# Kernel tuning notes

Measured on AMD Instinct MI355X. Metric: run time of the kernel, lower is better.

Reference implementation:

```python
import jax, jax.numpy as jnp
import numpy as np

N_NODES = 10000
N_EDGES = 80000
OBS_DIMS = 128
HIDDEN = 1024
ACT_DIMS = 8
N_GRAPHS = 64


def setup_inputs() -> dict:
    key = jax.random.key(0)
    ks = jax.random.split(key, 8)
    x = jax.random.normal(ks[0], (N_NODES, OBS_DIMS), dtype=jnp.float32)
    edge_index = jax.random.randint(ks[1], (2, N_EDGES), 0, N_NODES, dtype=jnp.int64)
    batch = jnp.sort(jax.random.randint(ks[2], (N_NODES,), 0, N_GRAPHS, dtype=jnp.int64))
    # Glorot-style init for weights, zero bias (as in PyG GCNConv / Linear defaults)
    W1 = jax.random.normal(ks[3], (OBS_DIMS, HIDDEN), dtype=jnp.float32) * (1.0 / np.sqrt(OBS_DIMS))
    b1 = jnp.zeros((HIDDEN,), dtype=jnp.float32)
    W2 = jax.random.normal(ks[4], (HIDDEN, HIDDEN), dtype=jnp.float32) * (1.0 / np.sqrt(HIDDEN))
    b2 = jnp.zeros((HIDDEN,), dtype=jnp.float32)
    Wl = jax.random.normal(ks[5], (HIDDEN, ACT_DIMS), dtype=jnp.float32) * (1.0 / np.sqrt(HIDDEN))
    bl = jnp.zeros((ACT_DIMS,), dtype=jnp.float32)
    return {"x": x, "edge_index": edge_index, "batch": batch,
            "W1": W1, "b1": b1, "W2": W2, "b2": b2, "Wl": Wl, "bl": bl}


def _gcn_conv(x, src, dst, dinv, W, b, n):
    """PyG GCNConv: D^-1/2 (A+I) D^-1/2 X W + b (self-loops already in src/dst)."""
    h = x @ W                                   # [N, out]
    norm = (dinv[src] * dinv[dst])[:, None]      # [E+N, 1]
    msg = h[src] * norm                          # gather + scale
    out = jax.ops.segment_sum(msg, dst, num_segments=n)
    return out + b


def reference(x, edge_index, batch, W1, b1, W2, b2, Wl, bl):
    n = x.shape[0]
    loops = jnp.arange(n, dtype=edge_index.dtype)
    src = jnp.concatenate([edge_index[0], loops])  # add self-loops
    dst = jnp.concatenate([edge_index[1], loops])
    # degree (with self-loops) from destination column, as PyG does
    deg = jax.ops.segment_sum(jnp.ones_like(dst, dtype=x.dtype), dst, num_segments=n)
    dinv = jax.lax.rsqrt(jnp.maximum(deg, 1.0))

    h = jax.nn.relu(_gcn_conv(x, src, dst, dinv, W1, b1, n))
    h = _gcn_conv(h, src, dst, dinv, W2, b2, n)
    h = jnp.tanh(h @ Wl + bl)                    # [N, act_dims]

    # global_mean_pool over batch segment ids
    sums = jax.ops.segment_sum(h, batch, num_segments=N_GRAPHS)
    counts = jax.ops.segment_sum(jnp.ones((n, 1), h.dtype), batch, num_segments=N_GRAPHS)
    return sums / jnp.maximum(counts, 1.0)       # [N_GRAPHS, act_dims]
```

## Files before the change

### kernel.cpp

```cpp
#include <hip/hip_runtime.h>
#include <hip/hip_bf16.h>

#define NNODES 10000
#define NEDGES 80000
#define OBS    128
#define HID    1024
#define ACTD   8
#define NGR    64

typedef __bf16 bf16x8 __attribute__((ext_vector_type(8)));
typedef float  f32x4  __attribute__((ext_vector_type(4)));
typedef const __attribute__((address_space(1))) unsigned int gl_u32;
typedef __attribute__((address_space(3))) unsigned int lds_u32;

__device__ __forceinline__ ushort f2b(float f) {
    union { float f; unsigned int i; } v; v.f = f;
    unsigned int lsb = (v.i >> 16) & 1u;
    unsigned int r = v.i + 0x7fffu + lsb;
    return (ushort)(r >> 16);
}
__device__ __forceinline__ int cix(int v, int hi) {
    return v < 0 ? 0 : (v >= hi ? hi - 1 : v);
}

__global__ __launch_bounds__(256) void k_prep(const float* __restrict__ W1,
                                              const float* __restrict__ W2,
                                              const float* __restrict__ Wl,
                                              const float* __restrict__ b2,
                                              const float* __restrict__ bl,
                                              ushort* __restrict__ Wt1,
                                              ushort* __restrict__ M2bf,
                                              float* __restrict__ b2l,
                                              float* __restrict__ zacc,
                                              float* __restrict__ pool,
                                              float* __restrict__ cnt,
                                              int* __restrict__ degi) {
    int blk = blockIdx.x;
    if (blk >= 385) {
        int idx = (blk - 385) * 256 + threadIdx.x;
        if (idx < NNODES * ACTD) zacc[idx] = 0.0f;
        if (idx < NGR * ACTD) pool[idx] = 0.0f;
        if (idx < NGR) cnt[idx] = 0.0f;
        if (idx < NNODES) degi[idx] = 0;
        return;
    }
    if (blk < 128) {
        __shared__ float tile[32][33];
        int bx = (blk & 31) * 32, by = (blk >> 5) * 32;
        int tx = threadIdx.x & 31, ty = threadIdx.x >> 5;
        #pragma unroll
        for (int i = 0; i < 32; i += 8)
            tile[ty + i][tx] = W1[(size_t)(by + ty + i) * HID + bx + tx];
        __syncthreads();
        #pragma unroll
        for (int i = 0; i < 32; i += 8)
            Wt1[(size_t)(bx + ty + i) * OBS + by + tx] = f2b(tile[tx][ty + i]);
        return;
    }
    int wvid = ((blk - 128) * 256 + (int)threadIdx.x) >> 6;
    int lane = threadIdx.x & 63;
    if (wvid > HID) return;
    const float* row = (wvid == HID) ? b2 : (W2 + (size_t)wvid * HID);
    float acc[ACTD];
    #pragma unroll
    for (int j = 0; j < ACTD; ++j) acc[j] = 0.0f;
    for (int it = 0; it < HID / 64; ++it) {
        int k = it * 64 + lane;
        float w2v = row[k];
        float4 a = *(const float4*)(Wl + (size_t)k * ACTD);
        float4 b = *(const float4*)(Wl + (size_t)k * ACTD + 4);
        acc[0] += w2v * a.x; acc[1] += w2v * a.y; acc[2] += w2v * a.z; acc[3] += w2v * a.w;
        acc[4] += w2v * b.x; acc[5] += w2v * b.y; acc[6] += w2v * b.z; acc[7] += w2v * b.w;
    }
    #pragma unroll
    for (int off = 32; off > 0; off >>= 1)
        #pragma unroll
        for (int j = 0; j < ACTD; ++j)
            acc[j] += __shfl_down(acc[j], off);
    if (lane == 0) {
        if (wvid == HID) {
            #pragma unroll
            for (int j = 0; j < ACTD; ++j) b2l[j] = acc[j] + bl[j];
        } else {
            #pragma unroll
            for (int j = 0; j < ACTD; ++j) M2bf[wvid * ACTD + j] = f2b(acc[j]);
        }
    }
}

__global__ void k_count(const int* __restrict__ dst, int* degi, int e) {
    int i = blockIdx.x * 256 + threadIdx.x;
    if (i < e) atomicAdd(&degi[cix(dst[i], NNODES)], 1);
}

__global__ __launch_bounds__(1024) void k_scan(const int* __restrict__ degi,
                                               int* rowptr, int* cursor, float* dinv) {
    __shared__ int wsum[16];
    int t = threadIdx.x, lane = t & 63, w = t >> 6;
    int base = t * 10;
    int local[10];
    int s = 0;
    #pragma unroll
    for (int k = 0; k < 10; ++k) {
        int i = base + k;
        int v = 0;
        if (i < NNODES) {
            v = degi[i];
            dinv[i] = rsqrtf((float)(v + 1));
        }
        local[k] = s; s += v;
    }
    int sc = s;
    #pragma unroll
    for (int off = 1; off < 64; off <<= 1) {
        int u = __shfl_up(sc, off);
        if (lane >= off) sc += u;
    }
    if (lane == 63) wsum[w] = sc;
    __syncthreads();
    if (w == 0 && lane < 16) {
        int v = wsum[lane];
        #pragma unroll
        for (int off = 1; off < 16; off <<= 1) {
            int u = __shfl_up(v, off);
            if (lane >= off) v += u;
        }
        wsum[lane] = v;
    }
    __syncthreads();
    int excl = ((w == 0) ? 0 : wsum[w - 1]) + (sc - s);
    #pragma unroll
    for (int k = 0; k < 10; ++k) {
        int i = base + k;
        if (i < NNODES) { rowptr[i] = excl + local[k]; cursor[i] = excl + local[k]; }
    }
    if (t == 0) rowptr[NNODES] = wsum[15];
}

__global__ void k_fill(const int* __restrict__ src, const int* __restrict__ dst,
                       const float* __restrict__ dinv, int* cursor,
                       int* __restrict__ esrc, float* __restrict__ coefs, int e) {
    int i = blockIdx.x * 256 + threadIdx.x;
    if (i >= e) return;
    int s = cix(src[i], NNODES), d = cix(dst[i], NNODES);
    int pos = atomicAdd(&cursor[d], 1);
    esrc[pos] = s;
    coefs[pos] = dinv[s] * dinv[d];
}

__global__ void k_aggx(const float* __restrict__ x, const float* __restrict__ dinv,
                       const int* __restrict__ rowptr, const int* __restrict__ esrc,
                       const float* __restrict__ coefs, ushort* __restrict__ aggbf, int n) {
    int wv = (blockIdx.x * 256 + threadIdx.x) >> 6;
    int lane = threadIdx.x & 63;
    if (wv >= n) return;
    float d = dinv[wv], d2 = d * d;
    float2 xv = *(const float2*)(x + (size_t)wv * OBS + lane * 2);
    float v0 = xv.x * d2, v1 = xv.y * d2;
    int e = rowptr[wv], e1 = rowptr[wv + 1];
    for (; e + 2 <= e1; e += 2) {
        int s0 = esrc[e], s1 = esrc[e + 1];
        float c0 = coefs[e], c1 = coefs[e + 1];
        float2 a = *(const float2*)(x + (size_t)s0 * OBS + lane * 2);
        float2 b = *(const float2*)(x + (size_t)s1 * OBS + lane * 2);
        v0 += a.x * c0 + b.x * c1;
        v1 += a.y * c0 + b.y * c1;
    }
    if (e < e1) {
        int s0 = esrc[e];
        float c0 = coefs[e];
        float2 a = *(const float2*)(x + (size_t)s0 * OBS + lane * 2);
        v0 += a.x * c0; v1 += a.y * c0;
    }
    ushort2 o; o.x = f2b(v0); o.y = f2b(v1);
    *(ushort2*)(aggbf + (size_t)wv * OBS + lane * 2) = o;
}

__global__ __launch_bounds__(256) void k_gemm1_fused(const ushort* __restrict__ A,
                                                     const ushort* __restrict__ Bt,
                                                     const float* __restrict__ bias,
                                                     const ushort* __restrict__ M2bf,
                                                     float* __restrict__ zacc,
                                                     int M) {
    __shared__ ushort buf[128 * 136 + 16 * 128];
    ushort* As    = buf;
    ushort* Bs    = buf + 8192;
    ushort* stage = buf;
    ushort* M2t   = buf + 128 * 136;

    const int t = threadIdx.x;
    const int bm = blockIdx.x, bn = blockIdx.y;
    const int lane = t & 63, wv = t >> 6;
    const int wm = (wv & 1) * 64, wn = (wv >> 1) * 64;
    const int l16 = lane & 15, kg = (lane >> 4) * 8;

    if (t < 128) {
        ushort4 a = *(const ushort4*)(M2bf + (size_t)(bn * 128 + t) * ACTD);
        ushort4 b = *(const ushort4*)(M2bf + (size_t)(bn * 128 + t) * ACTD + 4);
        M2t[0 * 128 + t] = a.x; M2t[1 * 128 + t] = a.y;
        M2t[2 * 128 + t] = a.z; M2t[3 * 128 + t] = a.w;
        M2t[4 * 128 + t] = b.x; M2t[5 * 128 + t] = b.y;
        M2t[6 * 128 + t] = b.z; M2t[7 * 128 + t] = b.w;
        #pragma unroll
        for (int j = 8; j < 16; ++j) M2t[j * 128 + t] = 0;
    }

    f32x4 acc[4][4];
    #pragma unroll
    for (int i = 0; i < 4; ++i)
        #pragma unroll
        for (int j = 0; j < 4; ++j)
            acc[i][j] = (f32x4){0.f, 0.f, 0.f, 0.f};

    const int rs = t >> 3;
    const int cs = (t & 7) * 8;
    #pragma unroll
    for (int kt = 0; kt < OBS; kt += 64) {
        #pragma unroll
        for (int p = 0; p < 4; ++p) {
            int r = rs + p * 32;
            int gr = bm * 128 + r; if (gr >= M) gr = M - 1;
            __builtin_amdgcn_global_load_lds(
                (gl_u32*)(A + (size_t)gr * OBS + kt + cs),
                (lds_u32*)(As + r * 64 + cs), 16, 0, 0);
            int gn = bn * 128 + r;
            __builtin_amdgcn_global_load_lds(
                (gl_u32*)(Bt + (size_t)gn * OBS + kt + cs),
                (lds_u32*)(Bs + r * 64 + cs), 16, 0, 0);
        }
        __syncthreads();
        #pragma unroll
        for (int k2 = 0; k2 < 64; k2 += 32) {
            bf16x8 af[4], bfr[4];
            #pragma unroll
            for (int i = 0; i < 4; ++i)
                af[i] = *(const bf16x8*)(As + (wm + i * 16 + l16) * 64 + k2 + kg);
            #pragma unroll
            for (int j = 0; j < 4; ++j)
                bfr[j] = *(const bf16x8*)(Bs + (wn + j * 16 + l16) * 64 + k2 + kg);
            #pragma unroll
            for (int i = 0; i < 4; ++i)
                #pragma unroll
                for (int j = 0; j < 4; ++j)
                    acc[i][j] = __builtin_amdgcn_mfma_f32_16x16x32_bf16(af[i], bfr[j], acc[i][j], 0, 0, 0);
        }
        __syncthreads();
    }

    #pragma unroll
    for (int i = 0; i < 4; ++i) {
        int rowb = wm + i * 16 + (lane >> 4) * 4;
        #pragma unroll
        for (int j = 0; j < 4; ++j) {
            int col = wn + j * 16 + l16;
            float bj = bias[bn * 128 + col];
            #pragma unroll
            for (int r = 0; r < 4; ++r)
                stage[(rowb + r) * 136 + col] = f2b(fmaxf(acc[i][j][r] + bj, 0.0f));
        }
    }
    __syncthreads();

    #pragma unroll
    for (int st = 0; st < 2; ++st) {
        int row0 = wv * 32 + st * 16;
        f32x4 z = (f32x4){0.f, 0.f, 0.f, 0.f};
        #pragma unroll
        for (int kt = 0; kt < 128; kt += 32) {
            bf16x8 a = *(const bf16x8*)(stage + (row0 + l16) * 136 + kt + kg);
            bf16x8 b = *(const bf16x8*)(M2t + l16 * 128 + kt + kg);
            z = __builtin_amdgcn_mfma_f32_16x16x32_bf16(a, b, z, 0, 0, 0);
        }
        if (l16 < ACTD) {
            int rowb = bm * 128 + row0 + (lane >> 4) * 4;
            #pragma unroll
            for (int r = 0; r < 4; ++r)
                if (rowb + r < M)
                    atomicAdd(&zacc[(size_t)(rowb + r) * ACTD + l16], z[r]);
        }
    }
}

__global__ __launch_bounds__(1024) void k_zfinal(const float* __restrict__ zacc,
                                                 const float* __restrict__ dinv,
                                                 const int* __restrict__ rowptr,
                                                 const int* __restrict__ esrc,
                                                 const float* __restrict__ coefs,
                                                 const float* __restrict__ b2l,
                                                 const int* __restrict__ batch,
                                                 float* __restrict__ pool,
                                                 float* __restrict__ cnt, int n) {
    __shared__ float part[NGR * ACTD];
    __shared__ int   partc[NGR];
    int t = threadIdx.x;
    if (t < NGR * ACTD) part[t] = 0.0f;
    if (t < NGR) partc[t] = 0;
    __syncthreads();

    int idx = blockIdx.x * 1024 + t;
    int i = idx >> 3, j = idx & 7;
    if (i < n) {
        float d = dinv[i];
        float v = zacc[idx] * d * d;
        int e0 = rowptr[i], e1 = rowptr[i + 1];
        for (int e = e0; e < e1; ++e)
            v += coefs[e] * zacc[(size_t)esrc[e] * ACTD + j];
        float tz = tanhf(v + b2l[j]);
        int g = cix(batch[i], NGR);
        atomicAdd(&part[g * ACTD + j], tz);
        if (j == 0) atomicAdd(&partc[g], 1);
    }
    __syncthreads();

    int i0 = (blockIdx.x * 1024) >> 3;
    int i1 = (blockIdx.x * 1024 + 1023) >> 3;
    if (i0 >= n) return;
    if (i1 >= n) i1 = n - 1;
    int g0 = cix(batch[i0], NGR), g1 = cix(batch[i1], NGR);
    int ng = g1 - g0 + 1;
    if (t < ng * ACTD)
        atomicAdd(&pool[g0 * ACTD + t], part[g0 * ACTD + t]);
    if (t < ng) {
        int c = partc[g0 + t];
        if (c) atomicAdd(&cnt[g0 + t], (float)c);
    }
}

__global__ void k_final(const float* __restrict__ pool, const float* __restrict__ cnt,
                        float* __restrict__ out, int total) {
    int i = blockIdx.x * 256 + threadIdx.x;
    if (i < total) out[i] = pool[i] / fmaxf(cnt[i >> 3], 1.0f);
}

extern "C" void kernel_launch(void* const* d_in, const int* in_sizes, int n_in,
                              void* d_out, int out_size, void* d_ws, size_t ws_size,
                              hipStream_t stream) {
    const float* x   = (const float*)d_in[0];
    const int*   ei  = (const int*)d_in[1];
    const int*   bat = (const int*)d_in[2];
    const float* W1  = (const float*)d_in[3];
    const float* b1  = (const float*)d_in[4];
    const float* W2  = (const float*)d_in[5];
    const float* b2v = (const float*)d_in[6];
    const float* Wl  = (const float*)d_in[7];
    const float* bl  = (const float*)d_in[8];
    float* out = (float*)d_out;

    const int N = NNODES, E = NEDGES;
    const int* src = ei;
    const int* dst = ei + E;

    char* ws = (char*)d_ws;
    size_t off = 0;
    float*  pool   = (float*)(ws + off); off += 2048;
    float*  cnt    = (float*)(ws + off); off += 256;
    float*  dinv   = (float*)(ws + off); off += 40192;
    int*    degi   = (int*)(ws + off);   off += 40192;
    int*    rowptr = (int*)(ws + off);   off += 40448;
    int*    cursor = (int*)(ws + off);   off += 40192;
    int*    esrc   = (int*)(ws + off);   off += (size_t)E * 4;
    float*  coefs  = (float*)(ws + off); off += (size_t)E * 4;
    float*  b2l    = (float*)(ws + off); off += 256;
    ushort* M2bf   = (ushort*)(ws + off); off += (size_t)HID * ACTD * 2;
    ushort* Wt1    = (ushort*)(ws + off); off += (size_t)HID * OBS * 2;
    float*  zacc   = (float*)(ws + off); off += (size_t)N * ACTD * 4;
    ushort* aggbf  = (ushort*)(ws + off); off += (size_t)N * OBS * 2;

    k_prep<<<698, 256, 0, stream>>>(W1, W2, Wl, b2v, bl, Wt1, M2bf, b2l,
                                    zacc, pool, cnt, degi);
    k_count<<<(E + 255) / 256, 256, 0, stream>>>(dst, degi, E);
    k_scan<<<1, 1024, 0, stream>>>(degi, rowptr, cursor, dinv);
    k_fill<<<(E + 255) / 256, 256, 0, stream>>>(src, dst, dinv, cursor, esrc, coefs, E);

    k_aggx<<<(N * 64 + 255) / 256, 256, 0, stream>>>(x, dinv, rowptr, esrc, coefs, aggbf, N);

    k_gemm1_fused<<<dim3((N + 127) / 128, HID / 128), 256, 0, stream>>>(
        aggbf, Wt1, b1, M2bf, zacc, N);

    k_zfinal<<<(N * ACTD + 1023) / 1024, 1024, 0, stream>>>(
        zacc, dinv, rowptr, esrc, coefs, b2l, bat, pool, cnt, N);
    k_final<<<2, 256, 0, stream>>>(pool, cnt, out, NGR * ACTD);
}
```

Measured before the change: 135.5 us.

## Fuse all pipeline stages into one cooperative persistent kernel with grid syncs

Replaces the eight separate kernel launches with a single cooperative kernel of 256 blocks of 512 threads, using grid.sync between stages (degree count, weight prep, scan, CSR fill, aggregation, fused GEMM, final aggregation and pooling). Workspace zeroing moves to a hipMemsetAsync over a contiguous region. The aim is to remove per-launch overhead and inter-kernel gaps. In exchange, each stage is limited to the persistent grid's parallelism, the GEMM tiles are processed in a grid-stride loop with a smaller per-wave tile, and every grid-wide barrier adds cost.

```diff
diff --git a/kernel.cpp b/kernel.cpp
--- a/kernel.cpp
+++ b/kernel.cpp
@@ -1,5 +1,6 @@
 #include <hip/hip_runtime.h>
 #include <hip/hip_bf16.h>
+#include <hip/hip_cooperative_groups.h>
 
 #define NNODES 10000
 #define NEDGES 80000
@@ -7,6 +8,10 @@
 #define HID    1024
 #define ACTD   8
 #define NGR    64
+#define NB     256
+#define NT     512
+
+namespace cg = cooperative_groups;
 
 typedef __bf16 bf16x8 __attribute__((ext_vector_type(8)));
 typedef float  f32x4  __attribute__((ext_vector_type(4)));
@@ -23,313 +28,282 @@
     return v < 0 ? 0 : (v >= hi ? hi - 1 : v);
 }
 
-__global__ __launch_bounds__(256) void k_prep(const float* __restrict__ W1,
-                                              const float* __restrict__ W2,
-                                              const float* __restrict__ Wl,
-                                              const float* __restrict__ b2,
-                                              const float* __restrict__ bl,
-                                              ushort* __restrict__ Wt1,
-                                              ushort* __restrict__ M2bf,
-                                              float* __restrict__ b2l,
-                                              float* __restrict__ zacc,
-                                              float* __restrict__ pool,
-                                              float* __restrict__ cnt,
-                                              int* __restrict__ degi) {
-    int blk = blockIdx.x;
-    if (blk >= 385) {
-        int idx = (blk - 385) * 256 + threadIdx.x;
-        if (idx < NNODES * ACTD) zacc[idx] = 0.0f;
-        if (idx < NGR * ACTD) pool[idx] = 0.0f;
-        if (idx < NGR) cnt[idx] = 0.0f;
-        if (idx < NNODES) degi[idx] = 0;
-        return;
-    }
-    if (blk < 128) {
-        __shared__ float tile[32][33];
-        int bx = (blk & 31) * 32, by = (blk >> 5) * 32;
-        int tx = threadIdx.x & 31, ty = threadIdx.x >> 5;
-        #pragma unroll
-        for (int i = 0; i < 32; i += 8)
-            tile[ty + i][tx] = W1[(size_t)(by + ty + i) * HID + bx + tx];
-        __syncthreads();
-        #pragma unroll
-        for (int i = 0; i < 32; i += 8)
-            Wt1[(size_t)(bx + ty + i) * OBS + by + tx] = f2b(tile[tx][ty + i]);
-        return;
-    }
-    int wvid = ((blk - 128) * 256 + (int)threadIdx.x) >> 6;
-    int lane = threadIdx.x & 63;
-    if (wvid > HID) return;
-    const float* row = (wvid == HID) ? b2 : (W2 + (size_t)wvid * HID);
-    float acc[ACTD];
-    #pragma unroll
-    for (int j = 0; j < ACTD; ++j) acc[j] = 0.0f;
-    for (int it = 0; it < HID / 64; ++it) {
-        int k = it * 64 + lane;
-        float w2v = row[k];
-        float4 a = *(const float4*)(Wl + (size_t)k * ACTD);
-        float4 b = *(const float4*)(Wl + (size_t)k * ACTD + 4);
-        acc[0] += w2v * a.x; acc[1] += w2v * a.y; acc[2] += w2v * a.z; acc[3] += w2v * a.w;
-        acc[4] += w2v * b.x; acc[5] += w2v * b.y; acc[6] += w2v * b.z; acc[7] += w2v * b.w;
-    }
-    #pragma unroll
-    for (int off = 32; off > 0; off >>= 1)
-        #pragma unroll
-        for (int j = 0; j < ACTD; ++j)
-            acc[j] += __shfl_down(acc[j], off);
-    if (lane == 0) {
-        if (wvid == HID) {
-            #pragma unroll
-            for (int j = 0; j < ACTD; ++j) b2l[j] = acc[j] + bl[j];
-        } else {
-            #pragma unroll
-            for (int j = 0; j < ACTD; ++j) M2bf[wvid * ACTD + j] = f2b(acc[j]);
-        }
-    }
-}
-
-__global__ void k_count(const int* __restrict__ dst, int* degi, int e) {
-    int i = blockIdx.x * 256 + threadIdx.x;
-    if (i < e) atomicAdd(&degi[cix(dst[i], NNODES)], 1);
-}
-
-__global__ __launch_bounds__(1024) void k_scan(const int* __restrict__ degi,
-                                               int* rowptr, int* cursor, float* dinv) {
-    __shared__ int wsum[16];
-    int t = threadIdx.x, lane = t & 63, w = t >> 6;
-    int base = t * 10;
-    int local[10];
-    int s = 0;
-    #pragma unroll
-    for (int k = 0; k < 10; ++k) {
-        int i = base + k;
-        int v = 0;
-        if (i < NNODES) {
-            v = degi[i];
-            dinv[i] = rsqrtf((float)(v + 1));
-        }
-        local[k] = s; s += v;
-    }
-    int sc = s;
-    #pragma unroll
-    for (int off = 1; off < 64; off <<= 1) {
-        int u = __shfl_up(sc, off);
-        if (lane >= off) sc += u;
-    }
-    if (lane == 63) wsum[w] = sc;
-    __syncthreads();
-    if (w == 0 && lane < 16) {
-        int v = wsum[lane];
-        #pragma unroll
-        for (int off = 1; off < 16; off <<= 1) {
-            int u = __shfl_up(v, off);
-            if (lane >= off) v += u;
-        }
-        wsum[lane] = v;
-    }
-    __syncthreads();
-    int excl = ((w == 0) ? 0 : wsum[w - 1]) + (sc - s);
-    #pragma unroll
-    for (int k = 0; k < 10; ++k) {
-        int i = base + k;
-        if (i < NNODES) { rowptr[i] = excl + local[k]; cursor[i] = excl + local[k]; }
-    }
-    if (t == 0) rowptr[NNODES] = wsum[15];
-}
-
-__global__ void k_fill(const int* __restrict__ src, const int* __restrict__ dst,
-                       const float* __restrict__ dinv, int* cursor,
-                       int* __restrict__ esrc, float* __restrict__ coefs, int e) {
-    int i = blockIdx.x * 256 + threadIdx.x;
-    if (i >= e) return;
-    int s = cix(src[i], NNODES), d = cix(dst[i], NNODES);
-    int pos = atomicAdd(&cursor[d], 1);
-    esrc[pos] = s;
-    coefs[pos] = dinv[s] * dinv[d];
-}
-
-__global__ void k_aggx(const float* __restrict__ x, const float* __restrict__ dinv,
-                       const int* __restrict__ rowptr, const int* __restrict__ esrc,
-                       const float* __restrict__ coefs, ushort* __restrict__ aggbf, int n) {
-    int wv = (blockIdx.x * 256 + threadIdx.x) >> 6;
-    int lane = threadIdx.x & 63;
-    if (wv >= n) return;
-    float d = dinv[wv], d2 = d * d;
-    float2 xv = *(const float2*)(x + (size_t)wv * OBS + lane * 2);
-    float v0 = xv.x * d2, v1 = xv.y * d2;
-    int e = rowptr[wv], e1 = rowptr[wv + 1];
-    for (; e + 2 <= e1; e += 2) {
-        int s0 = esrc[e], s1 = esrc[e + 1];
-        float c0 = coefs[e], c1 = coefs[e + 1];
-        float2 a = *(const float2*)(x + (size_t)s0 * OBS + lane * 2);
-        float2 b = *(const float2*)(x + (size_t)s1 * OBS + lane * 2);
-        v0 += a.x * c0 + b.x * c1;
-        v1 += a.y * c0 + b.y * c1;
-    }
-    if (e < e1) {
-        int s0 = esrc[e];
-        float c0 = coefs[e];
-        float2 a = *(const float2*)(x + (size_t)s0 * OBS + lane * 2);
-        v0 += a.x * c0; v1 += a.y * c0;
-    }
-    ushort2 o; o.x = f2b(v0); o.y = f2b(v1);
-    *(ushort2*)(aggbf + (size_t)wv * OBS + lane * 2) = o;
-}
-
-__global__ __launch_bounds__(256) void k_gemm1_fused(const ushort* __restrict__ A,
-                                                     const ushort* __restrict__ Bt,
-                                                     const float* __restrict__ bias,
-                                                     const ushort* __restrict__ M2bf,
-                                                     float* __restrict__ zacc,
-                                                     int M) {
+struct MegaArgs {
+    const float* x; const int* src; const int* dst; const int* bat;
+    const float* W1; const float* b1; const float* W2; const float* b2;
+    const float* Wl; const float* bl;
+    float* out;
+    float* pool; float* cnt; float* zacc; int* degi;
+    float* dinv; int* rowptr; int* cursor; int* esrc; float* coefs;
+    float* b2l; ushort* M2bf; ushort* Wt1; ushort* aggbf;
+};
+
+__global__ __launch_bounds__(NT, 2) void k_mega(MegaArgs a) {
+    cg::grid_group grid = cg::this_grid();
     __shared__ ushort buf[128 * 136 + 16 * 128];
-    ushort* As    = buf;
-    ushort* Bs    = buf + 8192;
-    ushort* stage = buf;
-    ushort* M2t   = buf + 128 * 136;
-
-    const int t = threadIdx.x;
-    const int bm = blockIdx.x, bn = blockIdx.y;
+    const int blk = blockIdx.x, t = threadIdx.x;
     const int lane = t & 63, wv = t >> 6;
-    const int wm = (wv & 1) * 64, wn = (wv >> 1) * 64;
-    const int l16 = lane & 15, kg = (lane >> 4) * 8;
-
-    if (t < 128) {
-        ushort4 a = *(const ushort4*)(M2bf + (size_t)(bn * 128 + t) * ACTD);
-        ushort4 b = *(const ushort4*)(M2bf + (size_t)(bn * 128 + t) * ACTD + 4);
-        M2t[0 * 128 + t] = a.x; M2t[1 * 128 + t] = a.y;
-        M2t[2 * 128 + t] = a.z; M2t[3 * 128 + t] = a.w;
-        M2t[4 * 128 + t] = b.x; M2t[5 * 128 + t] = b.y;
-        M2t[6 * 128 + t] = b.z; M2t[7 * 128 + t] = b.w;
-        #pragma unroll
-        for (int j = 8; j < 16; ++j) M2t[j * 128 + t] = 0;
-    }
-
-    f32x4 acc[4][4];
-    #pragma unroll
-    for (int i = 0; i < 4; ++i)
-        #pragma unroll
-        for (int j = 0; j < 4; ++j)
-            acc[i][j] = (f32x4){0.f, 0.f, 0.f, 0.f};
-
-    const int rs = t >> 3;
-    const int cs = (t & 7) * 8;
-    #pragma unroll
-    for (int kt = 0; kt < OBS; kt += 64) {
-        #pragma unroll
-        for (int p = 0; p < 4; ++p) {
-            int r = rs + p * 32;
-            int gr = bm * 128 + r; if (gr >= M) gr = M - 1;
-            __builtin_amdgcn_global_load_lds(
-                (gl_u32*)(A + (size_t)gr * OBS + kt + cs),
-                (lds_u32*)(As + r * 64 + cs), 16, 0, 0);
-            int gn = bn * 128 + r;
-            __builtin_amdgcn_global_load_lds(
-                (gl_u32*)(Bt + (size_t)gn * OBS + kt + cs),
-                (lds_u32*)(Bs + r * 64 + cs), 16, 0, 0);
-        }
-        __syncthreads();
-        #pragma unroll
-        for (int k2 = 0; k2 < 64; k2 += 32) {
-            bf16x8 af[4], bfr[4];
+
+    if (blk < 64) {
+        for (int i = blk * NT + t; i < NEDGES; i += 64 * NT)
+            atomicAdd(&a.degi[cix(a.dst[i], NNODES)], 1);
+    } else if (blk < 192) {
+        float* tile = (float*)buf;
+        int b2i = blk - 64;
+        int bx = (b2i & 31) * 32, by = (b2i >> 5) * 32;
+        int tx = t & 31, ty = t >> 5;
+        #pragma unroll
+        for (int i = 0; i < 32; i += 16)
+            tile[(ty + i) * 33 + tx] = a.W1[(size_t)(by + ty + i) * HID + bx + tx];
+        __syncthreads();
+        #pragma unroll
+        for (int i = 0; i < 32; i += 16)
+            a.Wt1[(size_t)(bx + ty + i) * OBS + by + tx] = f2b(tile[tx * 33 + ty + i]);
+    } else {
+        int w0 = (blk - 192) * 8 + wv;
+        for (int r = w0; r <= HID; r += 512) {
+            const float* row = (r == HID) ? a.b2 : (a.W2 + (size_t)r * HID);
+            float acc[ACTD];
+            #pragma unroll
+            for (int j = 0; j < ACTD; ++j) acc[j] = 0.0f;
+            for (int it = 0; it < HID / 64; ++it) {
+                int k = it * 64 + lane;
+                float w2v = row[k];
+                float4 p = *(const float4*)(a.Wl + (size_t)k * ACTD);
+                float4 q = *(const float4*)(a.Wl + (size_t)k * ACTD + 4);
+                acc[0] += w2v * p.x; acc[1] += w2v * p.y; acc[2] += w2v * p.z; acc[3] += w2v * p.w;
+                acc[4] += w2v * q.x; acc[5] += w2v * q.y; acc[6] += w2v * q.z; acc[7] += w2v * q.w;
+            }
+            #pragma unroll
+            for (int off = 32; off > 0; off >>= 1)
+                #pragma unroll
+                for (int j = 0; j < ACTD; ++j)
+                    acc[j] += __shfl_down(acc[j], off);
+            if (lane == 0) {
+                if (r == HID) {
+                    #pragma unroll
+                    for (int j = 0; j < ACTD; ++j) a.b2l[j] = acc[j] + a.bl[j];
+                } else {
+                    #pragma unroll
+                    for (int j = 0; j < ACTD; ++j) a.M2bf[r * ACTD + j] = f2b(acc[j]);
+                }
+            }
+        }
+    }
+    grid.sync();
+
+    if (blk == 0) {
+        int* wsum = (int*)buf;
+        int base = t * 20;
+        int local[20];
+        int s = 0;
+        #pragma unroll
+        for (int k = 0; k < 20; ++k) {
+            int i = base + k;
+            int v = 0;
+            if (i < NNODES) {
+                v = a.degi[i];
+                a.dinv[i] = rsqrtf((float)(v + 1));
+            }
+            local[k] = s; s += v;
+        }
+        int sc = s;
+        #pragma unroll
+        for (int off = 1; off < 64; off <<= 1) {
+            int u = __shfl_up(sc, off);
+            if (lane >= off) sc += u;
+        }
+        if (lane == 63) wsum[wv] = sc;
+        __syncthreads();
+        if (wv == 0 && lane < 8) {
+            int v = wsum[lane];
+            #pragma unroll
+            for (int off = 1; off < 8; off <<= 1) {
+                int u = __shfl_up(v, off);
+                if (lane >= off) v += u;
+            }
+            wsum[lane] = v;
+        }
+        __syncthreads();
+        int excl = ((wv == 0) ? 0 : wsum[wv - 1]) + (sc - s);
+        #pragma unroll
+        for (int k = 0; k < 20; ++k) {
+            int i = base + k;
+            if (i < NNODES) { a.rowptr[i] = excl + local[k]; a.cursor[i] = excl + local[k]; }
+        }
+        if (t == 0) a.rowptr[NNODES] = wsum[7];
+    }
+    grid.sync();
+
+    for (int i = blk * NT + t; i < NEDGES; i += NB * NT) {
+        int s = cix(a.src[i], NNODES), d = cix(a.dst[i], NNODES);
+        int pos = atomicAdd(&a.cursor[d], 1);
+        a.esrc[pos] = s;
+        a.coefs[pos] = a.dinv[s] * a.dinv[d];
+    }
+    grid.sync();
+
+    for (int nd = blk * 8 + wv; nd < NNODES; nd += NB * 8) {
+        float d = a.dinv[nd], d2 = d * d;
+        float2 xv = *(const float2*)(a.x + (size_t)nd * OBS + lane * 2);
+        float v0 = xv.x * d2, v1 = xv.y * d2;
+        int e = a.rowptr[nd], e1 = a.rowptr[nd + 1];
+        for (; e + 2 <= e1; e += 2) {
+            int s0 = a.esrc[e], s1 = a.esrc[e + 1];
+            float c0 = a.coefs[e], c1 = a.coefs[e + 1];
+            float2 p = *(const float2*)(a.x + (size_t)s0 * OBS + lane * 2);
+            float2 q = *(const float2*)(a.x + (size_t)s1 * OBS + lane * 2);
+            v0 += p.x * c0 + q.x * c1;
+            v1 += p.y * c0 + q.y * c1;
+        }
+        if (e < e1) {
+            int s0 = a.esrc[e];
+            float c0 = a.coefs[e];
+            float2 p = *(const float2*)(a.x + (size_t)s0 * OBS + lane * 2);
+            v0 += p.x * c0; v1 += p.y * c0;
+        }
+        ushort2 o; o.x = f2b(v0); o.y = f2b(v1);
+        *(ushort2*)(a.aggbf + (size_t)nd * OBS + lane * 2) = o;
+    }
+    grid.sync();
+
+    {
+        ushort* As    = buf;
+        ushort* Bs    = buf + 8192;
+        ushort* stage = buf;
+        ushort* M2t   = buf + 128 * 136;
+        const int wm = (wv & 1) * 64, wn = (wv >> 1) * 32;
+        const int l16 = lane & 15, kg = (lane >> 4) * 8;
+        const int rs = t >> 3;
+        const int cs = (t & 7) * 8;
+
+        for (int tile = blk; tile < 79 * 8; tile += NB) {
+            int bm = tile % 79, bn = tile / 79;
+            if (t < 128) {
+                ushort4 u = *(const ushort4*)(a.M2bf + (size_t)(bn * 128 + t) * ACTD);
+                ushort4 w = *(const ushort4*)(a.M2bf + (size_t)(bn * 128 + t) * ACTD + 4);
+                M2t[0 * 128 + t] = u.x; M2t[1 * 128 + t] = u.y;
+                M2t[2 * 128 + t] = u.z; M2t[3 * 128 + t] = u.w;
+                M2t[4 * 128 + t] = w.x; M2t[5 * 128 + t] = w.y;
+                M2t[6 * 128 + t] = w.z; M2t[7 * 128 + t] = w.w;
+                #pragma unroll
+                for (int j = 8; j < 16; ++j) M2t[j * 128 + t] = 0;
+            }
+            f32x4 acc[4][2];
             #pragma unroll
             for (int i = 0; i < 4; ++i)
-                af[i] = *(const bf16x8*)(As + (wm + i * 16 + l16) * 64 + k2 + kg);
-            #pragma unroll
-            for (int j = 0; j < 4; ++j)
-                bfr[j] = *(const bf16x8*)(Bs + (wn + j * 16 + l16) * 64 + k2 + kg);
-            #pragma unroll
-            for (int i = 0; i < 4; ++i)
-                #pragma unroll
-                for (int j = 0; j < 4; ++j)
-                    acc[i][j] = __builtin_amdgcn_mfma_f32_16x16x32_bf16(af[i], bfr[j], acc[i][j], 0, 0, 0);
-        }
-        __syncthreads();
-    }
-
-    #pragma unroll
-    for (int i = 0; i < 4; ++i) {
-        int rowb = wm + i * 16 + (lane >> 4) * 4;
-        #pragma unroll
-        for (int j = 0; j < 4; ++j) {
-            int col = wn + j * 16 + l16;
-            float bj = bias[bn * 128 + col];
-            #pragma unroll
-            for (int r = 0; r < 4; ++r)
-                stage[(rowb + r) * 136 + col] = f2b(fmaxf(acc[i][j][r] + bj, 0.0f));
-        }
-    }
-    __syncthreads();
-
-    #pragma unroll
-    for (int st = 0; st < 2; ++st) {
-        int row0 = wv * 32 + st * 16;
-        f32x4 z = (f32x4){0.f, 0.f, 0.f, 0.f};
-        #pragma unroll
-        for (int kt = 0; kt < 128; kt += 32) {
-            bf16x8 a = *(const bf16x8*)(stage + (row0 + l16) * 136 + kt + kg);
-            bf16x8 b = *(const bf16x8*)(M2t + l16 * 128 + kt + kg);
-            z = __builtin_amdgcn_mfma_f32_16x16x32_bf16(a, b, z, 0, 0, 0);
-        }
-        if (l16 < ACTD) {
-            int rowb = bm * 128 + row0 + (lane >> 4) * 4;
-            #pragma unroll
-            for (int r = 0; r < 4; ++r)
-                if (rowb + r < M)
-                    atomicAdd(&zacc[(size_t)(rowb + r) * ACTD + l16], z[r]);
-        }
-    }
-}
-
-__global__ __launch_bounds__(1024) void k_zfinal(const float* __restrict__ zacc,
-                                                 const float* __restrict__ dinv,
-                                                 const int* __restrict__ rowptr,
-                                                 const int* __restrict__ esrc,
-                                                 const float* __restrict__ coefs,
-                                                 const float* __restrict__ b2l,
-                                                 const int* __restrict__ batch,
-                                                 float* __restrict__ pool,
-                                                 float* __restrict__ cnt, int n) {
-    __shared__ float part[NGR * ACTD];
-    __shared__ int   partc[NGR];
-    int t = threadIdx.x;
-    if (t < NGR * ACTD) part[t] = 0.0f;
-    if (t < NGR) partc[t] = 0;
-    __syncthreads();
-
-    int idx = blockIdx.x * 1024 + t;
-    int i = idx >> 3, j = idx & 7;
-    if (i < n) {
-        float d = dinv[i];
-        float v = zacc[idx] * d * d;
-        int e0 = rowptr[i], e1 = rowptr[i + 1];
-        for (int e = e0; e < e1; ++e)
-            v += coefs[e] * zacc[(size_t)esrc[e] * ACTD + j];
-        float tz = tanhf(v + b2l[j]);
-        int g = cix(batch[i], NGR);
-        atomicAdd(&part[g * ACTD + j], tz);
-        if (j == 0) atomicAdd(&partc[g], 1);
-    }
-    __syncthreads();
-
-    int i0 = (blockIdx.x * 1024) >> 3;
-    int i1 = (blockIdx.x * 1024 + 1023) >> 3;
-    if (i0 >= n) return;
-    if (i1 >= n) i1 = n - 1;
-    int g0 = cix(batch[i0], NGR), g1 = cix(batch[i1], NGR);
-    int ng = g1 - g0 + 1;
-    if (t < ng * ACTD)
-        atomicAdd(&pool[g0 * ACTD + t], part[g0 * ACTD + t]);
-    if (t < ng) {
-        int c = partc[g0 + t];
-        if (c) atomicAdd(&cnt[g0 + t], (float)c);
-    }
-}
-
-__global__ void k_final(const float* __restrict__ pool, const float* __restrict__ cnt,
-                        float* __restrict__ out, int total) {
-    int i = blockIdx.x * 256 + threadIdx.x;
-    if (i < total) out[i] = pool[i] / fmaxf(cnt[i >> 3], 1.0f);
+                #pragma unroll
+                for (int j = 0; j < 2; ++j)
+                    acc[i][j] = (f32x4){0.f, 0.f, 0.f, 0.f};
+
+            #pragma unroll
+            for (int kt = 0; kt < OBS; kt += 64) {
+                #pragma unroll
+                for (int p = 0; p < 2; ++p) {
+                    int r = rs + p * 64;
+                    int gr = bm * 128 + r; if (gr >= NNODES) gr = NNODES - 1;
+                    __builtin_amdgcn_global_load_lds(
+                        (gl_u32*)(a.aggbf + (size_t)gr * OBS + kt + cs),
+                        (lds_u32*)(As + r * 64 + cs), 16, 0, 0);
+                    int gn = bn * 128 + r;
+                    __builtin_amdgcn_global_load_lds(
+                        (gl_u32*)(a.Wt1 + (size_t)gn * OBS + kt + cs),
+                        (lds_u32*)(Bs + r * 64 + cs), 16, 0, 0);
+                }
+                __syncthreads();
+                #pragma unroll
+                for (int k2 = 0; k2 < 64; k2 += 32) {
+                    bf16x8 af[4], bfr[2];
+                    #pragma unroll
+                    for (int i = 0; i < 4; ++i)
+                        af[i] = *(const bf16x8*)(As + (wm + i * 16 + l16) * 64 + k2 + kg);
+                    #pragma unroll
+                    for (int j = 0; j < 2; ++j)
+                        bfr[j] = *(const bf16x8*)(Bs + (wn + j * 16 + l16) * 64 + k2 + kg);
+                    #pragma unroll
+                    for (int i = 0; i < 4; ++i)
+                        #pragma unroll
+                        for (int j = 0; j < 2; ++j)
+                            acc[i][j] = __builtin_amdgcn_mfma_f32_16x16x32_bf16(af[i], bfr[j], acc[i][j], 0, 0, 0);
+                }
+                __syncthreads();
+            }
+
+            #pragma unroll
+            for (int i = 0; i < 4; ++i) {
+                int rowb = wm + i * 16 + (lane >> 4) * 4;
+                #pragma unroll
+                for (int j = 0; j < 2; ++j) {
+                    int col = wn + j * 16 + l16;
+                    float bj = a.b1[bn * 128 + col];
+                    #pragma unroll
+                    for (int r = 0; r < 4; ++r)
+                        stage[(rowb + r) * 136 + col] = f2b(fmaxf(acc[i][j][r] + bj, 0.0f));
+                }
+            }
+            __syncthreads();
+
+            {
+                int row0 = wv * 16;
+                f32x4 z = (f32x4){0.f, 0.f, 0.f, 0.f};
+                #pragma unroll
+                for (int kt = 0; kt < 128; kt += 32) {
+                    bf16x8 aa = *(const bf16x8*)(stage + (row0 + l16) * 136 + kt + kg);
+                    bf16x8 bb = *(const bf16x8*)(M2t + l16 * 128 + kt + kg);
+                    z = __builtin_amdgcn_mfma_f32_16x16x32_bf16(aa, bb, z, 0, 0, 0);
+                }
+                if (l16 < ACTD) {
+                    int rowb = bm * 128 + row0 + (lane >> 4) * 4;
+                    #pragma unroll
+                    for (int r = 0; r < 4; ++r)
+                        if (rowb + r < NNODES)
+                            atomicAdd(&a.zacc[(size_t)(rowb + r) * ACTD + l16], z[r]);
+                }
+            }
+            __syncthreads();
+        }
+    }
+    grid.sync();
+
+    {
+        float* part  = (float*)buf;
+        int*   partc = (int*)(buf + 1024);
+        if (t < NGR * ACTD) part[t] = 0.0f;
+        if (t < NGR) partc[t] = 0;
+        __syncthreads();
+        int i0 = blk * 40;
+        bool active = i0 < NNODES;
+        if (active && t < 40 * ACTD) {
+            int i = i0 + (t >> 3), j = t & 7;
+            if (i < NNODES) {
+                float d = a.dinv[i];
+                float v = a.zacc[(size_t)i * ACTD + j] * d * d;
+                int e0 = a.rowptr[i], e1 = a.rowptr[i + 1];
+                for (int e = e0; e < e1; ++e)
+                    v += a.coefs[e] * a.zacc[(size_t)a.esrc[e] * ACTD + j];
+                float tz = tanhf(v + a.b2l[j]);
+                int g = cix(a.bat[i], NGR);
+                atomicAdd(&part[g * ACTD + j], tz);
+                if (j == 0) atomicAdd(&partc[g], 1);
+            }
+        }
+        __syncthreads();
+        if (active) {
+            int i1 = i0 + 39; if (i1 >= NNODES) i1 = NNODES - 1;
+            int g0 = cix(a.bat[i0], NGR), g1 = cix(a.bat[i1], NGR);
+            int ng = g1 - g0 + 1;
+            if (t < ng * ACTD)
+                atomicAdd(&a.pool[g0 * ACTD + t], part[g0 * ACTD + t]);
+            if (t < ng) {
+                int c = partc[g0 + t];
+                if (c) atomicAdd(&a.cnt[g0 + t], (float)c);
+            }
+        }
+    }
+    grid.sync();
+
+    if (blk == 0 && t < NGR * ACTD)
+        a.out[t] = a.pool[t] / fmaxf(a.cnt[t >> 3], 1.0f);
 }
 
 extern "C" void kernel_launch(void* const* d_in, const int* in_sizes, int n_in,
@@ -346,38 +320,35 @@
     const float* bl  = (const float*)d_in[8];
     float* out = (float*)d_out;
 
-    const int N = NNODES, E = NEDGES;
-    const int* src = ei;
-    const int* dst = ei + E;
-
     char* ws = (char*)d_ws;
     size_t off = 0;
     float*  pool   = (float*)(ws + off); off += 2048;
     float*  cnt    = (float*)(ws + off); off += 256;
+    float*  zacc   = (float*)(ws + off); off += (size_t)NNODES * ACTD * 4;
+    int*    degi   = (int*)(ws + off);   off += 40192;
+    const size_t ZEROSZ = off;
     float*  dinv   = (float*)(ws + off); off += 40192;
-    int*    degi   = (int*)(ws + off);   off += 40192;
     int*    rowptr = (int*)(ws + off);   off += 40448;
     int*    cursor = (int*)(ws + off);   off += 40192;
-    int*    esrc   = (int*)(ws + off);   off += (size_t)E * 4;
-    float*  coefs  = (float*)(ws + off); off += (size_t)E * 4;
+    int*    esrc   = (int*)(ws + off);   off += (size_t)NEDGES * 4;
+    float*  coefs  = (float*)(ws + off); off += (size_t)NEDGES * 4;
     float*  b2l    = (float*)(ws + off); off += 256;
     ushort* M2bf   = (ushort*)(ws + off); off += (size_t)HID * ACTD * 2;
     ushort* Wt1    = (ushort*)(ws + off); off += (size_t)HID * OBS * 2;
-    float*  zacc   = (float*)(ws + off); off += (size_t)N * ACTD * 4;
-    ushort* aggbf  = (ushort*)(ws + off); off += (size_t)N * OBS * 2;
-
-    k_prep<<<698, 256, 0, stream>>>(W1, W2, Wl, b2v, bl, Wt1, M2bf, b2l,
-                                    zacc, pool, cnt, degi);
-    k_count<<<(E + 255) / 256, 256, 0, stream>>>(dst, degi, E);
-    k_scan<<<1, 1024, 0, stream>>>(degi, rowptr, cursor, dinv);
-    k_fill<<<(E + 255) / 256, 256, 0, stream>>>(src, dst, dinv, cursor, esrc, coefs, E);
-
-    k_aggx<<<(N * 64 + 255) / 256, 256, 0, stream>>>(x, dinv, rowptr, esrc, coefs, aggbf, N);
-
-    k_gemm1_fused<<<dim3((N + 127) / 128, HID / 128), 256, 0, stream>>>(
-        aggbf, Wt1, b1, M2bf, zacc, N);
-
-    k_zfinal<<<(N * ACTD + 1023) / 1024, 1024, 0, stream>>>(
-        zacc, dinv, rowptr, esrc, coefs, b2l, bat, pool, cnt, N);
-    k_final<<<2, 256, 0, stream>>>(pool, cnt, out, NGR * ACTD);
+    ushort* aggbf  = (ushort*)(ws + off); off += (size_t)NNODES * OBS * 2;
+
+    hipMemsetAsync(d_ws, 0, ZEROSZ, stream);
+
+    MegaArgs ar;
+    ar.x = x; ar.src = ei; ar.dst = ei + NEDGES; ar.bat = bat;
+    ar.W1 = W1; ar.b1 = b1; ar.W2 = W2; ar.b2 = b2v; ar.Wl = Wl; ar.bl = bl;
+    ar.out = out;
+    ar.pool = pool; ar.cnt = cnt; ar.zacc = zacc; ar.degi = degi;
+    ar.dinv = dinv; ar.rowptr = rowptr; ar.cursor = cursor;
+    ar.esrc = esrc; ar.coefs = coefs;
+    ar.b2l = b2l; ar.M2bf = M2bf; ar.Wt1 = Wt1; ar.aggbf = aggbf;
+
+    void* kparams[] = { &ar };
+    hipLaunchCooperativeKernel((const void*)k_mega, dim3(NB), dim3(NT),
+                               kparams, 0, stream);
 }
```

Result: slower. 332.3 us (+145.2%).

## Pack edge src/coef pairs, split aggregation across half-waves, fuse final division

Applied to the files above, without the earlier changes.

Edge source indices and coefficients are stored together as int2 pairs, so each edge costs one load instead of two. The x-aggregation kernel now splits each wave into two halves that process alternating edges with float4 loads, then combines the halves with a shuffle. The separate final normalization kernel is removed: the last block of k_zfinal, picked by an atomic ticket counter, writes the pooled means. This drops one launch and exposes more memory-level parallelism in the gather, at the cost of a threadfence/ticket scheme and divergent half-wave work.

```diff
diff --git a/kernel.cpp b/kernel.cpp
--- a/kernel.cpp
+++ b/kernel.cpp
@@ -34,6 +34,7 @@
                                               float* __restrict__ zacc,
                                               float* __restrict__ pool,
                                               float* __restrict__ cnt,
+                                              int* __restrict__ ticket,
                                               int* __restrict__ degi) {
     int blk = blockIdx.x;
     if (blk >= 385) {
@@ -42,6 +43,7 @@
         if (idx < NGR * ACTD) pool[idx] = 0.0f;
         if (idx < NGR) cnt[idx] = 0.0f;
         if (idx < NNODES) degi[idx] = 0;
+        if (idx == 0) *ticket = 0;
         return;
     }
     if (blk < 128) {
@@ -139,41 +141,53 @@
 
 __global__ void k_fill(const int* __restrict__ src, const int* __restrict__ dst,
                        const float* __restrict__ dinv, int* cursor,
-                       int* __restrict__ esrc, float* __restrict__ coefs, int e) {
+                       int2* __restrict__ epair, int e) {
     int i = blockIdx.x * 256 + threadIdx.x;
     if (i >= e) return;
     int s = cix(src[i], NNODES), d = cix(dst[i], NNODES);
     int pos = atomicAdd(&cursor[d], 1);
-    esrc[pos] = s;
-    coefs[pos] = dinv[s] * dinv[d];
+    epair[pos] = make_int2(s, __float_as_int(dinv[s] * dinv[d]));
 }
 
 __global__ void k_aggx(const float* __restrict__ x, const float* __restrict__ dinv,
-                       const int* __restrict__ rowptr, const int* __restrict__ esrc,
-                       const float* __restrict__ coefs, ushort* __restrict__ aggbf, int n) {
+                       const int* __restrict__ rowptr, const int2* __restrict__ epair,
+                       ushort* __restrict__ aggbf, int n) {
     int wv = (blockIdx.x * 256 + threadIdx.x) >> 6;
     int lane = threadIdx.x & 63;
     if (wv >= n) return;
-    float d = dinv[wv], d2 = d * d;
-    float2 xv = *(const float2*)(x + (size_t)wv * OBS + lane * 2);
-    float v0 = xv.x * d2, v1 = xv.y * d2;
-    int e = rowptr[wv], e1 = rowptr[wv + 1];
-    for (; e + 2 <= e1; e += 2) {
-        int s0 = esrc[e], s1 = esrc[e + 1];
-        float c0 = coefs[e], c1 = coefs[e + 1];
-        float2 a = *(const float2*)(x + (size_t)s0 * OBS + lane * 2);
-        float2 b = *(const float2*)(x + (size_t)s1 * OBS + lane * 2);
-        v0 += a.x * c0 + b.x * c1;
-        v1 += a.y * c0 + b.y * c1;
+    int half = lane >> 5, li = lane & 31;
+    float acc0 = 0.f, acc1 = 0.f, acc2 = 0.f, acc3 = 0.f;
+    if (half == 0) {
+        float d = dinv[wv], d2 = d * d;
+        float4 sv = *((const float4*)(x + (size_t)wv * OBS) + li);
+        acc0 = sv.x * d2; acc1 = sv.y * d2; acc2 = sv.z * d2; acc3 = sv.w * d2;
+    }
+    int e1 = rowptr[wv + 1];
+    int e = rowptr[wv] + half;
+    for (; e + 2 < e1; e += 4) {
+        int2 p0 = epair[e], p1 = epair[e + 2];
+        float c0 = __int_as_float(p0.y), c1 = __int_as_float(p1.y);
+        float4 a = *((const float4*)(x + (size_t)p0.x * OBS) + li);
+        float4 b = *((const float4*)(x + (size_t)p1.x * OBS) + li);
+        acc0 += a.x * c0 + b.x * c1;
+        acc1 += a.y * c0 + b.y * c1;
+        acc2 += a.z * c0 + b.z * c1;
+        acc3 += a.w * c0 + b.w * c1;
     }
     if (e < e1) {
-        int s0 = esrc[e];
-        float c0 = coefs[e];
-        float2 a = *(const float2*)(x + (size_t)s0 * OBS + lane * 2);
-        v0 += a.x * c0; v1 += a.y * c0;
-    }
-    ushort2 o; o.x = f2b(v0); o.y = f2b(v1);
-    *(ushort2*)(aggbf + (size_t)wv * OBS + lane * 2) = o;
+        int2 p0 = epair[e];
+        float c0 = __int_as_float(p0.y);
+        float4 a = *((const float4*)(x + (size_t)p0.x * OBS) + li);
+        acc0 += a.x * c0; acc1 += a.y * c0; acc2 += a.z * c0; acc3 += a.w * c0;
+    }
+    acc0 += __shfl_down(acc0, 32);
+    acc1 += __shfl_down(acc1, 32);
+    acc2 += __shfl_down(acc2, 32);
+    acc3 += __shfl_down(acc3, 32);
+    if (half == 0) {
+        ushort4 o; o.x = f2b(acc0); o.y = f2b(acc1); o.z = f2b(acc2); o.w = f2b(acc3);
+        *((ushort4*)(aggbf + (size_t)wv * OBS) + li) = o;
+    }
 }
 
 __global__ __launch_bounds__(256) void k_gemm1_fused(const ushort* __restrict__ A,
@@ -284,14 +298,16 @@
 __global__ __launch_bounds__(1024) void k_zfinal(const float* __restrict__ zacc,
                                                  const float* __restrict__ dinv,
                                                  const int* __restrict__ rowptr,
-                                                 const int* __restrict__ esrc,
-                                                 const float* __restrict__ coefs,
+                                                 const int2* __restrict__ epair,
                                                  const float* __restrict__ b2l,
                                                  const int* __restrict__ batch,
                                                  float* __restrict__ pool,
-                                                 float* __restrict__ cnt, int n) {
+                                                 float* __restrict__ cnt,
+                                                 int* __restrict__ ticket,
+                                                 float* __restrict__ out, int n) {
     __shared__ float part[NGR * ACTD];
     __shared__ int   partc[NGR];
+    __shared__ int   lastflag;
     int t = threadIdx.x;
     if (t < NGR * ACTD) part[t] = 0.0f;
     if (t < NGR) partc[t] = 0;
@@ -303,8 +319,10 @@
         float d = dinv[i];
         float v = zacc[idx] * d * d;
         int e0 = rowptr[i], e1 = rowptr[i + 1];
-        for (int e = e0; e < e1; ++e)
-            v += coefs[e] * zacc[(size_t)esrc[e] * ACTD + j];
+        for (int e = e0; e < e1; ++e) {
+            int2 p = epair[e];
+            v += __int_as_float(p.y) * zacc[(size_t)p.x * ACTD + j];
+        }
         float tz = tanhf(v + b2l[j]);
         int g = cix(batch[i], NGR);
         atomicAdd(&part[g * ACTD + j], tz);
@@ -314,22 +332,29 @@
 
     int i0 = (blockIdx.x * 1024) >> 3;
     int i1 = (blockIdx.x * 1024 + 1023) >> 3;
-    if (i0 >= n) return;
-    if (i1 >= n) i1 = n - 1;
-    int g0 = cix(batch[i0], NGR), g1 = cix(batch[i1], NGR);
-    int ng = g1 - g0 + 1;
-    if (t < ng * ACTD)
-        atomicAdd(&pool[g0 * ACTD + t], part[g0 * ACTD + t]);
-    if (t < ng) {
-        int c = partc[g0 + t];
-        if (c) atomicAdd(&cnt[g0 + t], (float)c);
-    }
-}
-
-__global__ void k_final(const float* __restrict__ pool, const float* __restrict__ cnt,
-                        float* __restrict__ out, int total) {
-    int i = blockIdx.x * 256 + threadIdx.x;
-    if (i < total) out[i] = pool[i] / fmaxf(cnt[i >> 3], 1.0f);
+    if (i0 < n) {
+        if (i1 >= n) i1 = n - 1;
+        int g0 = cix(batch[i0], NGR), g1 = cix(batch[i1], NGR);
+        int ng = g1 - g0 + 1;
+        if (t < ng * ACTD)
+            atomicAdd(&pool[g0 * ACTD + t], part[g0 * ACTD + t]);
+        if (t < ng) {
+            int c = partc[g0 + t];
+            if (c) atomicAdd(&cnt[g0 + t], (float)c);
+        }
+    }
+    __syncthreads();
+    if (t == 0) {
+        __threadfence();
+        int old = atomicAdd(ticket, 1);
+        lastflag = (old == (int)gridDim.x - 1);
+    }
+    __syncthreads();
+    if (lastflag && t < NGR * ACTD) {
+        float pv = atomicAdd(&pool[t], 0.0f);
+        float cv = atomicAdd(&cnt[t >> 3], 0.0f);
+        out[t] = pv / fmaxf(cv, 1.0f);
+    }
 }
 
 extern "C" void kernel_launch(void* const* d_in, const int* in_sizes, int n_in,
@@ -354,12 +379,12 @@
     size_t off = 0;
     float*  pool   = (float*)(ws + off); off += 2048;
     float*  cnt    = (float*)(ws + off); off += 256;
+    int*    ticket = (int*)(ws + off);   off += 256;
     float*  dinv   = (float*)(ws + off); off += 40192;
     int*    degi   = (int*)(ws + off);   off += 40192;
     int*    rowptr = (int*)(ws + off);   off += 40448;
     int*    cursor = (int*)(ws + off);   off += 40192;
-    int*    esrc   = (int*)(ws + off);   off += (size_t)E * 4;
-    float*  coefs  = (float*)(ws + off); off += (size_t)E * 4;
+    int2*   epair  = (int2*)(ws + off);  off += (size_t)E * 8;
     float*  b2l    = (float*)(ws + off); off += 256;
     ushort* M2bf   = (ushort*)(ws + off); off += (size_t)HID * ACTD * 2;
     ushort* Wt1    = (ushort*)(ws + off); off += (size_t)HID * OBS * 2;
@@ -367,17 +392,16 @@
     ushort* aggbf  = (ushort*)(ws + off); off += (size_t)N * OBS * 2;
 
     k_prep<<<698, 256, 0, stream>>>(W1, W2, Wl, b2v, bl, Wt1, M2bf, b2l,
-                                    zacc, pool, cnt, degi);
+                                    zacc, pool, cnt, ticket, degi);
     k_count<<<(E + 255) / 256, 256, 0, stream>>>(dst, degi, E);
     k_scan<<<1, 1024, 0, stream>>>(degi, rowptr, cursor, dinv);
-    k_fill<<<(E + 255) / 256, 256, 0, stream>>>(src, dst, dinv, cursor, esrc, coefs, E);
-
-    k_aggx<<<(N * 64 + 255) / 256, 256, 0, stream>>>(x, dinv, rowptr, esrc, coefs, aggbf, N);
+    k_fill<<<(E + 255) / 256, 256, 0, stream>>>(src, dst, dinv, cursor, epair, E);
+
+    k_aggx<<<(N * 64 + 255) / 256, 256, 0, stream>>>(x, dinv, rowptr, epair, aggbf, N);
 
     k_gemm1_fused<<<dim3((N + 127) / 128, HID / 128), 256, 0, stream>>>(
         aggbf, Wt1, b1, M2bf, zacc, N);
 
     k_zfinal<<<(N * ACTD + 1023) / 1024, 1024, 0, stream>>>(
-        zacc, dinv, rowptr, esrc, coefs, b2l, bat, pool, cnt, N);
-    k_final<<<2, 256, 0, stream>>>(pool, cnt, out, NGR * ACTD);
-}
+        zacc, dinv, rowptr, epair, b2l, bat, pool, cnt, ticket, out, N);
+}
```

Measured after the change: 138.3 us. 1.02x slower.
